# Kernel tuning notes

Measured on AMD Instinct MI355X. Metric: run time of the kernel, lower is better.

Reference implementation:

```python
import jax, jax.numpy as jnp
import numpy as np

EPS = 1e-8
N_BOXES = 500000


def _make_boxes(key, n):
    k1, k2, k3 = jax.random.split(key, 3)
    center = jax.random.uniform(k1, (n, 3), minval=-40.0, maxval=40.0)
    dims = jax.random.uniform(k2, (n, 3), minval=1.0, maxval=4.0)
    yaw = jax.random.uniform(k3, (n, 1), minval=-np.pi, maxval=np.pi)
    return jnp.concatenate([center, dims, yaw], axis=1).astype(jnp.float32)


def setup_inputs() -> dict:
    key = jax.random.key(0)
    kt, kc, kd, ky = jax.random.split(key, 4)
    target = _make_boxes(kt, N_BOXES)
    # pred = target + small perturbation so IoU is non-trivial
    dc = 0.3 * jax.random.normal(kc, (N_BOXES, 3))
    dd = jnp.exp(0.1 * jax.random.normal(kd, (N_BOXES, 3)))
    dy = 0.1 * jax.random.normal(ky, (N_BOXES, 1))
    pred = jnp.concatenate([target[:, :3] + dc,
                            target[:, 3:6] * dd,
                            target[:, 6:7] + dy], axis=1).astype(jnp.float32)
    weight = jnp.ones((N_BOXES,), dtype=jnp.float32)
    return {"pred": pred, "target": target, "weight": weight}


def box2corners(box):
    # box: (N,5) = (x, y, w, l, alpha) -> BEV corners (N,4,2)
    x, y, w, l, a = (box[:, i] for i in range(5))
    dx = jnp.array([0.5, -0.5, -0.5, 0.5], dtype=box.dtype)
    dy = jnp.array([0.5, 0.5, -0.5, -0.5], dtype=box.dtype)
    xs = dx[None, :] * w[:, None]
    ys = dy[None, :] * l[:, None]
    cos, sin = jnp.cos(a)[:, None], jnp.sin(a)[:, None]
    cx = x[:, None] + xs * cos - ys * sin
    cy = y[:, None] + xs * sin + ys * cos
    return jnp.stack([cx, cy], axis=-1)


def _cross2(a, b):
    return a[..., 0] * b[..., 1] - a[..., 1] * b[..., 0]


def box_intersection(c1, c2):
    # all 4x4 edge-pair intersections between two convex quads
    p1, p2 = c1, jnp.roll(c1, -1, axis=1)          # edges of box1
    q1, q2 = c2, jnp.roll(c2, -1, axis=1)          # edges of box2
    d1 = (p2 - p1)[:, :, None, :]                   # (N,4,1,2)
    d2 = (q2 - q1)[:, None, :, :]                   # (N,1,4,2)
    r = q1[:, None, :, :] - p1[:, :, None, :]       # (N,4,4,2)
    denom = _cross2(d1, d2)                         # (N,4,4)
    safe = jnp.where(jnp.abs(denom) < EPS, 1.0, denom)
    t = _cross2(r, d2) / safe
    u = _cross2(r, d1) / safe
    mask = (jnp.abs(denom) >= EPS) & (t > 0) & (t < 1) & (u > 0) & (u < 1)
    pts = p1[:, :, None, :] + t[..., None] * d1     # (N,4,4,2)
    pts = jnp.where(mask[..., None], pts, 0.0)
    n = c1.shape[0]
    return pts.reshape(n, 16, 2), mask.reshape(n, 16)


def points_in_box(pts, corners):
    # pts (N,4,2) inside rotated rect given by corners (N,4,2)
    a, b, d = corners[:, 0:1], corners[:, 1:2], corners[:, 3:4]
    ab, ad = b - a, d - a
    ap = pts - a
    pab = jnp.sum(ap * ab, -1) / jnp.sum(ab * ab, -1)
    pad = jnp.sum(ap * ad, -1) / jnp.sum(ad * ad, -1)
    e = 1e-6
    return (pab > -e) & (pab < 1 + e) & (pad > -e) & (pad < 1 + e)


def oriented_box_intersection_area(c1, c2):
    inter_pts, inter_mask = box_intersection(c1, c2)
    m1 = points_in_box(c1, c2)
    m2 = points_in_box(c2, c1)
    verts = jnp.concatenate([c1, c2, inter_pts], axis=1)   # (N,24,2)
    mask = jnp.concatenate([m1, m2, inter_mask], axis=1)   # (N,24)
    num = jnp.sum(mask, axis=1, keepdims=True)             # (N,1)
    mean = jnp.sum(verts * mask[..., None], axis=1, keepdims=True) / jnp.maximum(num, 1)[..., None]
    centered = verts - mean
    ang = jnp.arctan2(centered[..., 1], centered[..., 0])
    ang = jnp.where(mask, ang, 1e8)                        # invalid verts sort last
    idx = jnp.argsort(ang, axis=1)
    sv = jnp.take_along_axis(centered, idx[..., None], axis=1)
    sm = jnp.take_along_axis(mask, idx, axis=1)
    first = sv[:, 0:1, :]
    sv = jnp.where(sm[..., None], sv, first)               # pad with first valid vertex
    nxt = jnp.roll(sv, -1, axis=1)
    area = 0.5 * jnp.abs(jnp.sum(_cross2(sv, nxt), axis=1))
    return jnp.where(num[:, 0] > 2, area, 0.0)


def diff_iou_rotated_3d(box1, box2):
    # boxes: (N,7) = (x, y, z, w, l, h, alpha)
    c1 = box2corners(box1[:, jnp.array([0, 1, 3, 4, 6])])
    c2 = box2corners(box2[:, jnp.array([0, 1, 3, 4, 6])])
    inter_area = oriented_box_intersection_area(c1, c2)
    zmax = jnp.minimum(box1[:, 2] + 0.5 * box1[:, 5], box2[:, 2] + 0.5 * box2[:, 5])
    zmin = jnp.maximum(box1[:, 2] - 0.5 * box1[:, 5], box2[:, 2] - 0.5 * box2[:, 5])
    inter_vol = inter_area * jnp.clip(zmax - zmin, 0.0)
    v1 = box1[:, 3] * box1[:, 4] * box1[:, 5]
    v2 = box2[:, 3] * box2[:, 4] * box2[:, 5]
    return inter_vol / (v1 + v2 - inter_vol + EPS)


LOSS_WEIGHT = 1.0


def reference(pred, target, weight):
    iou = diff_iou_rotated_3d(pred, target)
    loss = (1.0 - iou) * weight
    return LOSS_WEIGHT * jnp.mean(loss)  # reduction='mean'
```

## Files before the change

### kernel.cpp

```cpp
#include <hip/hip_runtime.h>
#include <math.h>

#define NTH 256

__device__ __forceinline__ float frcp(float x) { return __builtin_amdgcn_rcpf(x); }

__device__ __forceinline__ float iou_loss_one(const float b1[7], const float b2[7], float w)
{
    float zmax = fminf(b1[2]+0.5f*b1[5], b2[2]+0.5f*b2[5]);
    float zmin = fmaxf(b1[2]-0.5f*b1[5], b2[2]-0.5f*b2[5]);
    float dz = fmaxf(zmax - zmin, 0.0f);
    float v1 = b1[3]*b1[4]*b1[5];
    float v2 = b2[3]*b2[4]*b2[5];

    float hw1 = 0.5f*b1[3], hl1 = 0.5f*b1[4];
    float hw2 = 0.5f*b2[3], hl2 = 0.5f*b2[4];

    float da = b2[6] - b1[6];
    float ct = __cosf(da), st = __sinf(da);
    float ca1 = __cosf(b1[6]), sa1 = __sinf(b1[6]);
    float ox = b2[0] - b1[0], oy = b2[1] - b1[1];
    float Ox =  ox*ca1 + oy*sa1;
    float Oy =  oy*ca1 - ox*sa1;

    float ux = hw2*ct, uy = hw2*st;
    float vx = -hl2*st, vy = hl2*ct;

    float wx_ = ux+vx, wy_ = uy+vy, zx_ = ux-vx, zy_ = uy-vy;
    float q0x = Ox+wx_, q0y = Oy+wy_;
    float q1x = Ox-zx_, q1y = Oy-zy_;
    float q2x = Ox-wx_, q2y = Oy-wy_;
    float q3x = Ox+zx_, q3y = Oy+zy_;

    float i2ux = frcp(ux+ux), i2uy = frcp(uy+uy);
    float i2vx = frcp(vx+vx), i2vy = frcp(vy+vy);

    float s2 = 0.0f;

    #define CLIP_Q(AX,AY,DX,DY,IUX,IUY)  {                                  \
        float ta = (-hw1 - (AX))*(IUX), tb = (hw1 - (AX))*(IUX);            \
        float tc = (-hl1 - (AY))*(IUY), td = (hl1 - (AY))*(IUY);            \
        float tlu = fminf(ta,tb), thu = fmaxf(ta,tb);                       \
        float tlv = fminf(tc,td), thv = fmaxf(tc,td);                       \
        float tin  = fmaxf(fmaxf(tlu,tlv), 0.0f);                           \
        float tout = fminf(fminf(thu,thv), 1.0f);                           \
        bool ok = tin < tout;                                               \
        float Apx = (AX) + tin*(DX),  Apy = (AY) + tin*(DY);                \
        float Bpx = (AX) + tout*(DX), Bpy = (AY) + tout*(DY);               \
        float cr = Apx*Bpy - Apy*Bpx;                                       \
        s2 += ok ? cr : 0.0f; }

    CLIP_Q(q0x,q0y, -(ux+ux), -(uy+uy), -i2ux, -i2uy)
    CLIP_Q(q1x,q1y, -(vx+vx), -(vy+vy), -i2vx, -i2vy)
    CLIP_Q(q2x,q2y,  (ux+ux),  (uy+uy),  i2ux,  i2uy)
    CLIP_Q(q3x,q3y,  (vx+vx),  (vy+vy),  i2vx,  i2vy)
    #undef CLIP_Q

    #define PROJ(PX,PY,PU,PV) { float rx=(PX)-Ox, ry=(PY)-Oy;               \
        PU = rx*ct + ry*st;  PV = ry*ct - rx*st; }
    float p0u,p0v,p1u,p1v,p2u,p2v,p3u,p3v;
    PROJ( hw1,  hl1, p0u,p0v)
    PROJ(-hw1,  hl1, p1u,p1v)
    PROJ(-hw1, -hl1, p2u,p2v)
    PROJ( hw1, -hl1, p3u,p3v)
    #undef PROJ

    float Au = (hw1+hw1)*ct, Av = (hw1+hw1)*st;
    float Cu = (hl1+hl1)*st, Cv = (hl1+hl1)*ct;
    float iAu = frcp(Au), iAv = frcp(Av), iCu = frcp(Cu), iCv = frcp(Cv);

    float sdt = 0.0f;
    #define CLIP_P(PU,PV,IDU,IDV) {                                         \
        float ta = (-hw2 - (PU))*(IDU), tb = (hw2 - (PU))*(IDU);            \
        float tc = (-hl2 - (PV))*(IDV), td = (hl2 - (PV))*(IDV);            \
        float tlu = fminf(ta,tb), thu = fmaxf(ta,tb);                       \
        float tlv = fminf(tc,td), thv = fmaxf(tc,td);                       \
        float tin  = fmaxf(fmaxf(tlu,tlv), 0.0f);                           \
        float tout = fminf(fminf(thu,thv), 1.0f);                           \
        float dt = tout - tin;                                              \
        sdt += (dt > 0.0f) ? dt : 0.0f; }

    CLIP_P(p0u,p0v, -iAu,  iAv)
    CLIP_P(p1u,p1v, -iCu, -iCv)
    CLIP_P(p2u,p2v,  iAu, -iAv)
    CLIP_P(p3u,p3v,  iCu,  iCv)
    #undef CLIP_P

    s2 += (hw1+hw1)*hl1*sdt;

    float area = 0.5f*fabsf(s2);
    float inter_vol = area * dz;
    float iou = inter_vol * frcp(v1 + v2 - inter_vol + 1e-8f);
    return (1.0f - iou) * w;
}

__global__ __launch_bounds__(NTH) void iou_loss_kernel(
    const float* __restrict__ pred, const float* __restrict__ target,
    const float* __restrict__ weight, float* __restrict__ partial, int n)
{
    int i = blockIdx.x * blockDim.x + threadIdx.x;
    float loss = 0.0f;
    if (i < n) {
        float b1[7], b2[7];
        #pragma unroll
        for (int j = 0; j < 7; ++j) { b1[j] = pred[i*7+j]; b2[j] = target[i*7+j]; }
        loss = iou_loss_one(b1, b2, weight[i]);
    }

    #pragma unroll
    for (int off = 32; off > 0; off >>= 1) loss += __shfl_down(loss, off, 64);
    __shared__ float wsum[NTH/64];
    int lane = threadIdx.x & 63, wid = threadIdx.x >> 6;
    if (lane == 0) wsum[wid] = loss;
    __syncthreads();
    if (threadIdx.x == 0) {
        float s = 0.0f;
        #pragma unroll
        for (int w = 0; w < NTH/64; ++w) s += wsum[w];
        partial[blockIdx.x] = s;
    }
}

__global__ __launch_bounds__(NTH) void reduce_kernel(
    const float* __restrict__ partial, int nb, float* __restrict__ out, double inv_n)
{
    double s = 0.0;
    for (int j = threadIdx.x; j < nb; j += NTH) s += (double)partial[j];
    #pragma unroll
    for (int off = 32; off > 0; off >>= 1) s += __shfl_down(s, off, 64);
    __shared__ double wsum[NTH/64];
    int lane = threadIdx.x & 63, wid = threadIdx.x >> 6;
    if (lane == 0) wsum[wid] = s;
    __syncthreads();
    if (threadIdx.x == 0) {
        double tot = 0.0;
        #pragma unroll
        for (int w = 0; w < NTH/64; ++w) tot += wsum[w];
        out[0] = (float)(tot * inv_n);
    }
}

extern "C" void kernel_launch(void* const* d_in, const int* in_sizes, int n_in,
                              void* d_out, int out_size, void* d_ws, size_t ws_size,
                              hipStream_t stream) {
    const float* pred   = (const float*)d_in[0];
    const float* target = (const float*)d_in[1];
    const float* weight = (const float*)d_in[2];
    int n = in_sizes[2];
    float* partial = (float*)d_ws;
    int nblocks = (n + NTH - 1) / NTH;
    hipLaunchKernelGGL(iou_loss_kernel, dim3(nblocks), dim3(NTH), 0, stream,
                       pred, target, weight, partial, n);
    hipLaunchKernelGGL(reduce_kernel, dim3(1), dim3(NTH), 0, stream,
                       partial, nblocks, (float*)d_out, 1.0 / (double)n);
}
```

Measured before the change: 13.42 us.

## Process four rows per thread with prefetch and simplify trig and corner projection

Each thread now handles four boxes, and the loads for the next box are issued before computing the current one, so memory latency overlaps with arithmetic. The grid shrinks fourfold, which also means fewer partial sums for the reduce kernel. The relative yaw cos/sin are now built from each box's own cos/sin by angle-difference identities, and the projected box1 corners are derived incrementally from one projected corner. The trade-offs are higher register pressure, fewer blocks to fill the GPU, and slightly different rounding.

```diff
diff --git a/kernel.cpp b/kernel.cpp
--- a/kernel.cpp
+++ b/kernel.cpp
@@ -2,6 +2,8 @@
 #include <math.h>
 
 #define NTH 256
+#define G   4
+#define RPB (NTH*G)
 
 __device__ __forceinline__ float frcp(float x) { return __builtin_amdgcn_rcpf(x); }
 
@@ -16,9 +18,10 @@
     float hw1 = 0.5f*b1[3], hl1 = 0.5f*b1[4];
     float hw2 = 0.5f*b2[3], hl2 = 0.5f*b2[4];
 
-    float da = b2[6] - b1[6];
-    float ct = __cosf(da), st = __sinf(da);
     float ca1 = __cosf(b1[6]), sa1 = __sinf(b1[6]);
+    float ca2 = __cosf(b2[6]), sa2 = __sinf(b2[6]);
+    float ct = ca2*ca1 + sa2*sa1;
+    float st = sa2*ca1 - ca2*sa1;
     float ox = b2[0] - b1[0], oy = b2[1] - b1[1];
     float Ox =  ox*ca1 + oy*sa1;
     float Oy =  oy*ca1 - ox*sa1;
@@ -56,18 +59,15 @@
     CLIP_Q(q3x,q3y,  (vx+vx),  (vy+vy),  i2vx,  i2vy)
     #undef CLIP_Q
 
-    #define PROJ(PX,PY,PU,PV) { float rx=(PX)-Ox, ry=(PY)-Oy;               \
-        PU = rx*ct + ry*st;  PV = ry*ct - rx*st; }
-    float p0u,p0v,p1u,p1v,p2u,p2v,p3u,p3v;
-    PROJ( hw1,  hl1, p0u,p0v)
-    PROJ(-hw1,  hl1, p1u,p1v)
-    PROJ(-hw1, -hl1, p2u,p2v)
-    PROJ( hw1, -hl1, p3u,p3v)
-    #undef PROJ
-
     float Au = (hw1+hw1)*ct, Av = (hw1+hw1)*st;
     float Cu = (hl1+hl1)*st, Cv = (hl1+hl1)*ct;
     float iAu = frcp(Au), iAv = frcp(Av), iCu = frcp(Cu), iCv = frcp(Cv);
+
+    float rx = hw1 - Ox, ry = hl1 - Oy;
+    float p0u = rx*ct + ry*st,  p0v = ry*ct - rx*st;
+    float p1u = p0u - Au, p1v = p0v + Av;
+    float p2u = p1u - Cu, p2v = p1v - Cv;
+    float p3u = p0u - Cu, p3v = p0v - Cv;
 
     float sdt = 0.0f;
     #define CLIP_P(PU,PV,IDU,IDV) {                                         \
@@ -98,22 +98,43 @@
     const float* __restrict__ pred, const float* __restrict__ target,
     const float* __restrict__ weight, float* __restrict__ partial, int n)
 {
-    int i = blockIdx.x * blockDim.x + threadIdx.x;
+    const int tid = threadIdx.x;
+    const int row0 = blockIdx.x * RPB;
     float loss = 0.0f;
-    if (i < n) {
-        float b1[7], b2[7];
+
+    float b1[G][7], b2[G][7], wv[G];
+    #define LOADG(g, i) {                                                   \
+        _Pragma("unroll")                                                   \
+        for (int j = 0; j < 7; ++j) {                                       \
+            b1[g][j] = pred[(i)*7+j]; b2[g][j] = target[(i)*7+j]; }         \
+        wv[g] = weight[i]; }
+
+    if (row0 + RPB <= n) {
+        LOADG(0, row0 + tid)
         #pragma unroll
-        for (int j = 0; j < 7; ++j) { b1[j] = pred[i*7+j]; b2[j] = target[i*7+j]; }
-        loss = iou_loss_one(b1, b2, weight[i]);
+        for (int g = 0; g < G; ++g) {
+            if (g + 1 < G) LOADG(g + 1, row0 + (g + 1) * NTH + tid)
+            loss += iou_loss_one(b1[g], b2[g], wv[g]);
+        }
+    } else {
+        #pragma unroll
+        for (int g = 0; g < G; ++g) {
+            int i = row0 + g * NTH + tid;
+            if (i < n) {
+                LOADG(g, i)
+                loss += iou_loss_one(b1[g], b2[g], wv[g]);
+            }
+        }
     }
+    #undef LOADG
 
     #pragma unroll
     for (int off = 32; off > 0; off >>= 1) loss += __shfl_down(loss, off, 64);
     __shared__ float wsum[NTH/64];
-    int lane = threadIdx.x & 63, wid = threadIdx.x >> 6;
+    int lane = tid & 63, wid = tid >> 6;
     if (lane == 0) wsum[wid] = loss;
     __syncthreads();
-    if (threadIdx.x == 0) {
+    if (tid == 0) {
         float s = 0.0f;
         #pragma unroll
         for (int w = 0; w < NTH/64; ++w) s += wsum[w];
@@ -148,7 +169,7 @@
     const float* weight = (const float*)d_in[2];
     int n = in_sizes[2];
     float* partial = (float*)d_ws;
-    int nblocks = (n + NTH - 1) / NTH;
+    int nblocks = (n + RPB - 1) / RPB;
     hipLaunchKernelGGL(iou_loss_kernel, dim3(nblocks), dim3(NTH), 0, stream,
                        pred, target, weight, partial, n);
     hipLaunchKernelGGL(reduce_kernel, dim3(1), dim3(NTH), 0, stream,
```

Result: faster. 13.10 us (-2.4%).
